# Kernel optimization log

Hardware: AMD Instinct MI355X
Metric: run time of the kernel (lower is better)

## Reference

```python
import jax, jax.numpy as jnp
import numpy as np

N_NODES = 512      # num_nodes (seq_len for LSTM, also output side length)
B = 64             # graph batch -> total nodes = B * N_NODES
T = B * N_NODES    # 32768 total nodes
E = 1048576        # edges before self-loops
D_IN = 128
H = 128
L = 2              # lstm layers


def setup_inputs() -> dict:
    key = jax.random.key(0)
    ks = jax.random.split(key, 12)
    x = jax.random.normal(ks[0], (T, D_IN), dtype=jnp.float32)
    edge_index = jax.random.randint(ks[1], (2, E), 0, T, dtype=jnp.int64)
    edge_weight = jax.random.uniform(ks[2], (E,), dtype=jnp.float32)
    batch = jax.random.randint(ks[3], (T,), 0, B, dtype=jnp.int64)
    s = 1.0 / np.sqrt(H)
    W_gcn = jax.random.normal(ks[4], (D_IN, H), dtype=jnp.float32) * s
    b_gcn = jnp.zeros((H,), dtype=jnp.float32)
    w_ih = jax.random.uniform(ks[5], (L, 4 * H, H), minval=-s, maxval=s, dtype=jnp.float32)
    w_hh = jax.random.uniform(ks[6], (L, 4 * H, H), minval=-s, maxval=s, dtype=jnp.float32)
    b_ih = jax.random.uniform(ks[7], (L, 4 * H), minval=-s, maxval=s, dtype=jnp.float32)
    b_hh = jax.random.uniform(ks[8], (L, 4 * H), minval=-s, maxval=s, dtype=jnp.float32)
    fc_w = jax.random.uniform(ks[9], (N_NODES * N_NODES, H), minval=-s, maxval=s, dtype=jnp.float32)
    fc_b = jax.random.uniform(ks[10], (N_NODES * N_NODES,), minval=-s, maxval=s, dtype=jnp.float32)
    return {"x": x, "edge_index": edge_index, "edge_weight": edge_weight, "batch": batch,
            "W_gcn": W_gcn, "b_gcn": b_gcn, "w_ih": w_ih, "w_hh": w_hh,
            "b_ih": b_ih, "b_hh": b_hh, "fc_w": fc_w, "fc_b": fc_b}


def _gcn_conv(x, edge_index, edge_weight, W, b):
    # PyG GCNConv with edge weights: add self-loops (w=1), symmetric norm, then aggregate.
    n = x.shape[0]
    loop = jnp.arange(n, dtype=edge_index.dtype)
    src = jnp.concatenate([edge_index[0], loop])
    dst = jnp.concatenate([edge_index[1], loop])
    w = jnp.concatenate([edge_weight, jnp.ones((n,), dtype=edge_weight.dtype)])
    deg = jax.ops.segment_sum(w, dst, num_segments=n)
    dinv = jnp.where(deg > 0, jax.lax.rsqrt(jnp.maximum(deg, 1e-30)), 0.0)
    norm = dinv[src] * w * dinv[dst]                  # [E+n]
    xw = x @ W                                        # [n, H]
    msg = norm[:, None] * xw[src]                     # gather + scale
    out = jax.ops.segment_sum(msg, dst, num_segments=n)  # scatter-add
    return out + b


def _lstm_layer(xs, wih, whh, bih, bhh):
    # xs: [S, B, H] time-major; torch gate order i,f,g,o.
    h0 = jnp.zeros((xs.shape[1], whh.shape[1]), dtype=xs.dtype)
    c0 = jnp.zeros_like(h0)
    def step(carry, xt):
        h, c = carry
        gates = xt @ wih.T + h @ whh.T + bih + bhh
        i, f, g, o = jnp.split(gates, 4, axis=-1)
        c = jax.nn.sigmoid(f) * c + jax.nn.sigmoid(i) * jnp.tanh(g)
        h = jax.nn.sigmoid(o) * jnp.tanh(c)
        return (h, c), h
    _, hs = jax.lax.scan(step, (h0, c0), xs)
    return hs


def reference(x, edge_index, edge_weight, batch, W_gcn, b_gcn, w_ih, w_hh, b_ih, b_hh, fc_w, fc_b):
    h = _gcn_conv(x, edge_index, edge_weight, W_gcn, b_gcn)   # [T, H]
    # split into chunks of num_nodes and stack -> [B, N_NODES, H]
    h = h.reshape(B, N_NODES, H)
    xs = jnp.transpose(h, (1, 0, 2))                           # [S, B, H]
    for l in range(L):
        xs = _lstm_layer(xs, w_ih[l], w_hh[l], b_ih[l], b_hh[l])
    last = xs[-1]                                              # [B, H]
    out = last @ fc_w.T + fc_b                                 # [B, N_NODES^2]
    return out.reshape(N_NODES, -1)
```

## Files before the change

### kernel.cpp

```cpp
#include <hip/hip_runtime.h>

#define TNODES 32768
#define NEDGE  1048576
#define HD     128
#define NG     512
#define NB     64
#define SEQ    512
#define FCN    262144

__global__ __launch_bounds__(256) void k_deg(const int* __restrict__ ei,
                                             const float* __restrict__ ew,
                                             float* __restrict__ deg,
                                             int* __restrict__ cnt) {
    int e = blockIdx.x * 256 + threadIdx.x;
    int d = ei[NEDGE + e];
    atomicAdd(&deg[d], ew[e]);
    atomicAdd(&cnt[d], 1);
}

__global__ __launch_bounds__(256) void k_dinv(float* __restrict__ deg) {
    int n = blockIdx.x * 256 + threadIdx.x;
    deg[n] = rsqrtf(deg[n] + 1.0f);
}

__global__ __launch_bounds__(1024) void k_scan(const int* __restrict__ cnt,
                                               int* __restrict__ offs) {
    __shared__ int sums[1024];
    int t = threadIdx.x;
    int base = t * 32;
    int local[32];
    int s = 0;
    #pragma unroll
    for (int j = 0; j < 32; ++j) { local[j] = s; s += cnt[base + j]; }
    sums[t] = s;
    __syncthreads();
    for (int off = 1; off < 1024; off <<= 1) {
        int v = sums[t];
        int u = (t >= off) ? sums[t - off] : 0;
        __syncthreads();
        sums[t] = v + u;
        __syncthreads();
    }
    int baseSum = (t == 0) ? 0 : sums[t - 1];
    #pragma unroll
    for (int j = 0; j < 32; ++j) offs[base + j] = baseSum + local[j];
    if (t == 1023) offs[TNODES] = sums[1023];
}

__global__ __launch_bounds__(256) void k_fill(const int* __restrict__ ei,
                                              const float* __restrict__ ew,
                                              const float* __restrict__ dinv,
                                              const int* __restrict__ offs,
                                              int* __restrict__ cursor,
                                              int* __restrict__ csrc,
                                              float* __restrict__ ca) {
    int e = blockIdx.x * 256 + threadIdx.x;
    int s = ei[e];
    int d = ei[NEDGE + e];
    int p = offs[d] + atomicAdd(&cursor[d], 1);
    csrc[p] = s;
    ca[p] = ew[e] * dinv[s];
}

__global__ __launch_bounds__(256) void k_transpose(const float* __restrict__ W,
                                                   float* __restrict__ Wt) {
    int t = blockIdx.x * 256 + threadIdx.x;
    int c = t >> 7, k = t & 127;
    Wt[t] = W[k * HD + c];
}

#define GS 140
__global__ __launch_bounds__(256) void k_gemm_bt(const float* __restrict__ A,
                                                 const float* __restrict__ Bt,
                                                 const float* __restrict__ b1,
                                                 const float* __restrict__ b2,
                                                 float* __restrict__ C, int G) {
    __shared__ __align__(16) float As[64 * GS];
    __shared__ __align__(16) float Bs[64 * GS];
    int r0 = blockIdx.x * 64;
    int g0 = blockIdx.y * 64;
    int tid = threadIdx.x;
    #pragma unroll
    for (int it = 0; it < 8; ++it) {
        int idx = tid + 256 * it;
        int r = idx >> 5, c4 = idx & 31;
        float4 va = ((const float4*)(A + (size_t)(r0 + r) * HD))[c4];
        *((float4*)&As[r * GS + c4 * 4]) = va;
        float4 vb = ((const float4*)(Bt + (size_t)(g0 + r) * HD))[c4];
        *((float4*)&Bs[r * GS + c4 * 4]) = vb;
    }
    __syncthreads();
    int i = tid >> 4;
    int j = tid & 15;
    float acc[4][4];
    #pragma unroll
    for (int a = 0; a < 4; ++a)
        #pragma unroll
        for (int b = 0; b < 4; ++b) acc[a][b] = 0.f;
    #pragma unroll 8
    for (int k4 = 0; k4 < 32; ++k4) {
        float4 av[4], bv[4];
        #pragma unroll
        for (int mi = 0; mi < 4; ++mi)
            av[mi] = *((const float4*)&As[(i + 16 * mi) * GS + k4 * 4]);
        #pragma unroll
        for (int ni = 0; ni < 4; ++ni)
            bv[ni] = *((const float4*)&Bs[(j + 16 * ni) * GS + k4 * 4]);
        #pragma unroll
        for (int mi = 0; mi < 4; ++mi)
            #pragma unroll
            for (int ni = 0; ni < 4; ++ni)
                acc[mi][ni] += (av[mi].x * bv[ni].x + av[mi].y * bv[ni].y) +
                               (av[mi].z * bv[ni].z + av[mi].w * bv[ni].w);
    }
    #pragma unroll
    for (int mi = 0; mi < 4; ++mi)
        #pragma unroll
        for (int ni = 0; ni < 4; ++ni) {
            int g = g0 + j + 16 * ni;
            float bias = (b1 ? b1[g] : 0.f) + (b2 ? b2[g] : 0.f);
            C[(size_t)(r0 + i + 16 * mi) * G + g] = acc[mi][ni] + bias;
        }
}

__global__ __launch_bounds__(128) void k_agg(const int* __restrict__ offs,
                                             const int* __restrict__ csrc,
                                             const float* __restrict__ ca,
                                             const float* __restrict__ xw,
                                             const float* __restrict__ dinv,
                                             const float* __restrict__ bg,
                                             float* __restrict__ hg) {
    int d = blockIdx.x;
    int t = threadIdx.x;
    int beg = offs[d], end = offs[d + 1];
    float acc = 0.f;
    int e = beg;
    for (; e + 3 < end; e += 4) {
        int s0 = csrc[e], s1 = csrc[e + 1], s2 = csrc[e + 2], s3 = csrc[e + 3];
        float a0 = ca[e], a1 = ca[e + 1], a2 = ca[e + 2], a3 = ca[e + 3];
        acc += a0 * xw[(size_t)s0 * HD + t];
        acc += a1 * xw[(size_t)s1 * HD + t];
        acc += a2 * xw[(size_t)s2 * HD + t];
        acc += a3 * xw[(size_t)s3 * HD + t];
    }
    for (; e < end; ++e) acc += ca[e] * xw[(size_t)csrc[e] * HD + t];
    float di = dinv[d];
    hg[(size_t)d * HD + t] = di * acc + di * di * xw[(size_t)d * HD + t] + bg[t];
}

__device__ __forceinline__ float sigm(float x) { return 1.f / (1.f + __expf(-x)); }
__device__ __forceinline__ float tanh_s(float x) {
    float e = __expf(-2.f * fabsf(x));
    float t = (1.f - e) / (1.f + e);
    return copysignf(t, x);
}

#define COMP(v, j) ((j) == 0 ? (v).x : ((j) == 1 ? (v).y : ((j) == 2 ? (v).z : (v).w)))

__global__ __launch_bounds__(512)
__attribute__((amdgpu_waves_per_eu(2, 2)))
void k_lstm(const float* __restrict__ P,
            const float* __restrict__ whh,
            float* __restrict__ Hout,
            float* __restrict__ lastOut) {
    __shared__ __align__(16) float lds[20608];
    float* h_sh = lds + 2048;
    int b = blockIdx.x, t = threadIdx.x;
    int c = t >> 7;
    int i = t & 127;

    float4 w[4][8];
    for (int g = 0; g < 4; ++g) {
        for (int h8 = 0; h8 < 8; ++h8) {
            int rl = t >> 5;
            int kq = (t & 31) * 4;
            float4 v = *(const float4*)(whh + (size_t)(128 * g + 16 * h8 + rl) * HD + kq);
            __syncthreads();
            *(float4*)(lds + 4 * t) = v;
            __syncthreads();
            if ((i >> 4) == h8) {
                int rr = i & 15;
                #pragma unroll
                for (int q = 0; q < 8; ++q)
                    w[g][q] = *(const float4*)(lds + rr * 128 + 32 * c + 4 * q);
            }
        }
    }
    __syncthreads();

    if (t < HD) h_sh[t] = 0.f;
    float cst = 0.f;
    const float* Pb = P + (size_t)b * SEQ * NG;
    float pi = 0.f, pf = 0.f, pg = 0.f, po = 0.f;
    if (t < HD) { pi = Pb[t]; pf = Pb[128 + t]; pg = Pb[256 + t]; po = Pb[384 + t]; }
    __syncthreads();

    for (int s = 0; s < SEQ; ++s) {
        float pi2 = 0.f, pf2 = 0.f, pg2 = 0.f, po2 = 0.f;
        if (t < HD && s + 1 < SEQ) {
            const float* Pn = Pb + (size_t)(s + 1) * NG;
            pi2 = Pn[t]; pf2 = Pn[128 + t]; pg2 = Pn[256 + t]; po2 = Pn[384 + t];
        }
        float hv = h_sh[32 * c + (t & 31)];
        float4 acc = {0.f, 0.f, 0.f, 0.f};
        #pragma unroll
        for (int k = 0; k < 32; ++k) {
            float h = __int_as_float(__builtin_amdgcn_readlane(__float_as_int(hv), k));
            acc.x = fmaf(COMP(w[0][k >> 2], k & 3), h, acc.x);
            acc.y = fmaf(COMP(w[1][k >> 2], k & 3), h, acc.y);
            acc.z = fmaf(COMP(w[2][k >> 2], k & 3), h, acc.z);
            acc.w = fmaf(COMP(w[3][k >> 2], k & 3), h, acc.w);
        }
        ((float4*)lds)[c * 128 + i] = acc;
        __syncthreads();

        if (t < HD) {
            float4 s0 = ((const float4*)lds)[t];
            float4 s1 = ((const float4*)lds)[128 + t];
            float4 s2 = ((const float4*)lds)[256 + t];
            float4 s3 = ((const float4*)lds)[384 + t];
            float gi = (s0.x + s1.x) + (s2.x + s3.x) + pi;
            float gf = (s0.y + s1.y) + (s2.y + s3.y) + pf;
            float gg = (s0.z + s1.z) + (s2.z + s3.z) + pg;
            float go = (s0.w + s1.w) + (s2.w + s3.w) + po;
            float i_ = sigm(gi), f_ = sigm(gf), g_ = tanh_s(gg), o_ = sigm(go);
            cst = fmaf(f_, cst, i_ * g_);
            float h = o_ * tanh_s(cst);
            h_sh[t] = h;
            if (Hout) Hout[((size_t)b * SEQ + s) * HD + t] = h;
            if (lastOut && s == SEQ - 1) lastOut[b * HD + t] = h;
        }
        pi = pi2; pf = pf2; pg = pg2; po = po2;
        __syncthreads();
    }
}

__global__ __launch_bounds__(256) void k_fc(const float* __restrict__ last,
                                            const float* __restrict__ fcw,
                                            const float* __restrict__ fcb,
                                            float* __restrict__ out) {
    __shared__ __align__(16) float l_sh[NB * HD];
    int tid = threadIdx.x;
    #pragma unroll
    for (int it = 0; it < 32; ++it) l_sh[tid + 256 * it] = last[tid + 256 * it];
    __syncthreads();
    int i = blockIdx.x * 256 + tid;
    const float4* wrow = (const float4*)(fcw + (size_t)i * HD);
    float acc[NB];
    #pragma unroll
    for (int b = 0; b < NB; ++b) acc[b] = 0.f;
    for (int k4 = 0; k4 < 32; ++k4) {
        float4 w4 = wrow[k4];
        #pragma unroll
        for (int b = 0; b < NB; ++b) {
            float4 l4 = ((const float4*)(l_sh + b * HD))[k4];
            acc[b] += (w4.x * l4.x + w4.y * l4.y) + (w4.z * l4.z + w4.w * l4.w);
        }
    }
    float bias = fcb[i];
    #pragma unroll
    for (int b = 0; b < NB; ++b) out[(size_t)b * FCN + i] = acc[b] + bias;
}

extern "C" void kernel_launch(void* const* d_in, const int* in_sizes, int n_in,
                              void* d_out, int out_size, void* d_ws, size_t ws_size,
                              hipStream_t stream) {
    const float* x   = (const float*)d_in[0];
    const int*   ei  = (const int*)d_in[1];
    const float* ew  = (const float*)d_in[2];
    const float* Wg  = (const float*)d_in[4];
    const float* bg  = (const float*)d_in[5];
    const float* wih = (const float*)d_in[6];
    const float* whh = (const float*)d_in[7];
    const float* bih = (const float*)d_in[8];
    const float* bhh = (const float*)d_in[9];
    const float* fcw = (const float*)d_in[10];
    const float* fcb = (const float*)d_in[11];
    float* out = (float*)d_out;

    float* ws = (float*)d_ws;
    float* deg    = ws;
    int*   cnt    = (int*)(ws + 32768);
    int*   cursor = (int*)(ws + 65536);
    int*   offs   = (int*)(ws + 98304);
    int*   csrc   = (int*)(ws + 131136);
    float* ca     = ws + 1179712;
    float* Wt     = ws + 2228288;
    float* xw     = ws + 2244672;
    float* hg     = ws + 6438976;
    float* H0     = ws + 10633280;
    float* lastb  = ws + 14827584;
    float* P      = ws + 14835776;

    hipMemsetAsync(d_ws, 0, 3 * 32768 * sizeof(float), stream);

    k_deg<<<NEDGE / 256, 256, 0, stream>>>(ei, ew, deg, cnt);
    k_dinv<<<TNODES / 256, 256, 0, stream>>>(deg);
    k_scan<<<1, 1024, 0, stream>>>(cnt, offs);
    k_fill<<<NEDGE / 256, 256, 0, stream>>>(ei, ew, deg, offs, cursor, csrc, ca);
    k_transpose<<<64, 256, 0, stream>>>(Wg, Wt);
    k_gemm_bt<<<dim3(TNODES / 64, HD / 64), 256, 0, stream>>>(x, Wt, nullptr, nullptr, xw, HD);
    k_agg<<<TNODES, 128, 0, stream>>>(offs, csrc, ca, xw, deg, bg, hg);

    k_gemm_bt<<<dim3(TNODES / 64, NG / 64), 256, 0, stream>>>(hg, wih, bih, bhh, P, NG);
    k_lstm<<<NB, 512, 0, stream>>>(P, whh, H0, nullptr);
    k_gemm_bt<<<dim3(TNODES / 64, NG / 64), 256, 0, stream>>>(H0, wih + 65536, bih + 512, bhh + 512, P, NG);
    k_lstm<<<NB, 512, 0, stream>>>(P, whh + 65536, nullptr, lastb);

    k_fc<<<FCN / 256, 256, 0, stream>>>(lastb, fcw, fcb, out);
}
```

Baseline: 1.655 ms.

## Make all LSTM threads compute gates redundantly and double-buffer partials to drop a barrier

Measured after the change: 1.763 ms. 6.5% more time.

```diff
diff --git a/kernel.cpp b/kernel.cpp
--- a/kernel.cpp
+++ b/kernel.cpp
@@ -164,10 +164,10 @@
             float* __restrict__ Hout,
             float* __restrict__ lastOut) {
     __shared__ __align__(16) float lds[20608];
-    float* h_sh = lds + 2048;
     int b = blockIdx.x, t = threadIdx.x;
     int c = t >> 7;
     int i = t & 127;
+    int u = 32 * c + (t & 31);
 
     float4 w[4][8];
     for (int g = 0; g < 4; ++g) {
@@ -187,50 +187,47 @@
         }
     }
     __syncthreads();
-
-    if (t < HD) h_sh[t] = 0.f;
+    ((float4*)lds)[t] = float4{0.f, 0.f, 0.f, 0.f};
+
     float cst = 0.f;
     const float* Pb = P + (size_t)b * SEQ * NG;
-    float pi = 0.f, pf = 0.f, pg = 0.f, po = 0.f;
-    if (t < HD) { pi = Pb[t]; pf = Pb[128 + t]; pg = Pb[256 + t]; po = Pb[384 + t]; }
+    float pi = Pb[u], pf = Pb[128 + u], pg = Pb[256 + u], po = Pb[384 + u];
     __syncthreads();
 
     for (int s = 0; s < SEQ; ++s) {
         float pi2 = 0.f, pf2 = 0.f, pg2 = 0.f, po2 = 0.f;
-        if (t < HD && s + 1 < SEQ) {
+        if (s + 1 < SEQ) {
             const float* Pn = Pb + (size_t)(s + 1) * NG;
-            pi2 = Pn[t]; pf2 = Pn[128 + t]; pg2 = Pn[256 + t]; po2 = Pn[384 + t];
-        }
-        float hv = h_sh[32 * c + (t & 31)];
-        float4 acc = {0.f, 0.f, 0.f, 0.f};
-        #pragma unroll
-        for (int k = 0; k < 32; ++k) {
-            float h = __int_as_float(__builtin_amdgcn_readlane(__float_as_int(hv), k));
-            acc.x = fmaf(COMP(w[0][k >> 2], k & 3), h, acc.x);
-            acc.y = fmaf(COMP(w[1][k >> 2], k & 3), h, acc.y);
-            acc.z = fmaf(COMP(w[2][k >> 2], k & 3), h, acc.z);
-            acc.w = fmaf(COMP(w[3][k >> 2], k & 3), h, acc.w);
-        }
-        ((float4*)lds)[c * 128 + i] = acc;
-        __syncthreads();
-
-        if (t < HD) {
-            float4 s0 = ((const float4*)lds)[t];
-            float4 s1 = ((const float4*)lds)[128 + t];
-            float4 s2 = ((const float4*)lds)[256 + t];
-            float4 s3 = ((const float4*)lds)[384 + t];
-            float gi = (s0.x + s1.x) + (s2.x + s3.x) + pi;
-            float gf = (s0.y + s1.y) + (s2.y + s3.y) + pf;
-            float gg = (s0.z + s1.z) + (s2.z + s3.z) + pg;
-            float go = (s0.w + s1.w) + (s2.w + s3.w) + po;
-            float i_ = sigm(gi), f_ = sigm(gf), g_ = tanh_s(gg), o_ = sigm(go);
-            cst = fmaf(f_, cst, i_ * g_);
-            float h = o_ * tanh_s(cst);
-            h_sh[t] = h;
-            if (Hout) Hout[((size_t)b * SEQ + s) * HD + t] = h;
-            if (lastOut && s == SEQ - 1) lastOut[b * HD + t] = h;
-        }
+            pi2 = Pn[u]; pf2 = Pn[128 + u]; pg2 = Pn[256 + u]; po2 = Pn[384 + u];
+        }
+        const float4* buf = ((const float4*)lds) + (s & 1) * 512;
+        float4 q0 = buf[u];
+        float4 q1 = buf[128 + u];
+        float4 q2 = buf[256 + u];
+        float4 q3 = buf[384 + u];
+        float gi = (q0.x + q1.x) + (q2.x + q3.x) + pi;
+        float gf = (q0.y + q1.y) + (q2.y + q3.y) + pf;
+        float gg = (q0.z + q1.z) + (q2.z + q3.z) + pg;
+        float go = (q0.w + q1.w) + (q2.w + q3.w) + po;
+        float i_ = sigm(gi), f_ = sigm(gf), g_ = tanh_s(gg), o_ = sigm(go);
+        cst = fmaf(f_, cst, i_ * g_);
+        float h = o_ * tanh_s(cst);
+        if (Hout && (t & 96) == 0) Hout[((size_t)b * SEQ + s) * HD + u] = h;
+        if (lastOut && s == SEQ - 1 && (t & 96) == 0) lastOut[b * HD + u] = h;
         pi = pi2; pf = pf2; pg = pg2; po = po2;
+
+        if (s + 1 < SEQ) {
+            float4 acc = {0.f, 0.f, 0.f, 0.f};
+            #pragma unroll
+            for (int k = 0; k < 32; ++k) {
+                float hk = __int_as_float(__builtin_amdgcn_readlane(__float_as_int(h), k));
+                acc.x = fmaf(COMP(w[0][k >> 2], k & 3), hk, acc.x);
+                acc.y = fmaf(COMP(w[1][k >> 2], k & 3), hk, acc.y);
+                acc.z = fmaf(COMP(w[2][k >> 2], k & 3), hk, acc.z);
+                acc.w = fmaf(COMP(w[3][k >> 2], k & 3), hk, acc.w);
+            }
+            ((float4*)lds)[((s + 1) & 1) * 512 + c * 128 + i] = acc;
+        }
         __syncthreads();
     }
 }
```
